# Performance work log

Hardware: AMD Instinct MI355X
Metric: run time of the kernel (lower is better)

## Reference

```python
import jax, jax.numpy as jnp
import numpy as np

B, T, C = 4, 2048, 1024
H = 16
DH = C // H  # 64


def setup_inputs() -> dict:
    key = jax.random.key(0)
    ks = jax.random.split(key, 6)
    s = 1.0 / np.sqrt(C)
    x = jax.random.normal(ks[0], (B, T, C), dtype=jnp.float32)
    # per-head projection weights, stacked: (H, C, DH)
    Wq = jax.random.uniform(ks[1], (H, C, DH), dtype=jnp.float32, minval=-s, maxval=s)
    Wk = jax.random.uniform(ks[2], (H, C, DH), dtype=jnp.float32, minval=-s, maxval=s)
    Wv = jax.random.uniform(ks[3], (H, C, DH), dtype=jnp.float32, minval=-s, maxval=s)
    # output projection (torch Linear: y = x @ W.T + b); store as (C, C) for x @ Wo
    Wo = jax.random.uniform(ks[4], (C, C), dtype=jnp.float32, minval=-s, maxval=s)
    bo = jax.random.uniform(ks[5], (C,), dtype=jnp.float32, minval=-s, maxval=s)
    return {"x": x, "Wq": Wq, "Wk": Wk, "Wv": Wv, "Wo": Wo, "bo": bo}


def reference(x, Wq, Wk, Wv, Wo, bo):
    # x: (B,T,C) -> q,k,v: (B,H,T,DH)
    q = jnp.einsum('btc,hcd->bhtd', x, Wq)
    k = jnp.einsum('btc,hcd->bhtd', x, Wk)
    v = jnp.einsum('btc,hcd->bhtd', x, Wv)
    scale = DH ** -0.5
    scores = jnp.einsum('bhtd,bhsd->bhts', q, k) * scale  # (B,H,T,T)
    causal = jnp.tril(jnp.ones((T, T), dtype=bool))
    scores = jnp.where(causal, scores, -jnp.inf)
    wei = jax.nn.softmax(scores, axis=-1)
    out = jnp.einsum('bhts,bhsd->bhtd', wei, v)  # (B,H,T,DH)
    # concat heads: (B,T,H*DH) = (B,T,C)
    out = out.transpose(0, 2, 1, 3).reshape(B, T, C)
    return out @ Wo + bo
```

## Files before the change

kernel.cpp:

```cpp
#include <hip/hip_runtime.h>

#define T_SEQ 2048
#define C_DIM 1024
#define H_NUM 16
#define DHD   64
#define B_NUM 4
#define M_ROWS (B_NUM*T_SEQ)

typedef __bf16 bf16x8 __attribute__((ext_vector_type(8)));
typedef float  f32x4  __attribute__((ext_vector_type(4)));
typedef unsigned short ushort8 __attribute__((ext_vector_type(8)));
typedef unsigned short ushort4e __attribute__((ext_vector_type(4)));

__device__ __forceinline__ unsigned short f2b(float f){
  return __builtin_bit_cast(unsigned short, (__bf16)f);
}
__device__ __forceinline__ bf16x8 as_bf(ushort8 u){ return __builtin_bit_cast(bf16x8, u); }
__device__ __forceinline__ float exp2fast(float x){ return __builtin_amdgcn_exp2f(x); }

__device__ __forceinline__ void gload16(const void* g, void* l){
  __builtin_amdgcn_global_load_lds(
      (const __attribute__((address_space(1))) void*)g,
      (__attribute__((address_space(3))) void*)l, 16, 0, 0);
}

__global__ __launch_bounds__(256) void k_conv_x(const float* __restrict__ x,
                                                unsigned short* __restrict__ xb){
  int i = blockIdx.x*256 + threadIdx.x;
  float4 f = ((const float4*)x)[i];
  ushort4e o;
  o[0]=f2b(f.x); o[1]=f2b(f.y); o[2]=f2b(f.z); o[3]=f2b(f.w);
  ((ushort4e*)xb)[i] = o;
}

__global__ __launch_bounds__(256) void k_pack_w(const float* __restrict__ wq,
                                                const float* __restrict__ wk,
                                                const float* __restrict__ wv,
                                                const float* __restrict__ wo,
                                                unsigned short* __restrict__ wt,
                                                unsigned short* __restrict__ wot){
  int idx = blockIdx.x*256 + threadIdx.x;
  if (idx < 3*C_DIM*C_DIM){
    int nall = idx >> 10; int c = idx & 1023;
    int m = nall >> 10;   int n = nall & 1023;
    int h = n >> 6, d = n & 63;
    const float* w = (m==0) ? wq : (m==1) ? wk : wv;
    float f = w[((size_t)h*C_DIM + c)*DHD + d];
    if (m == 0) f *= 0.125f * 1.4426950408889634f;
    wt[idx] = f2b(f);
  } else {
    int j = idx - 3*C_DIM*C_DIM;
    int n = j >> 10, c = j & 1023;
    wot[j] = f2b(wo[(size_t)c*C_DIM + n]);
  }
}

__global__ __launch_bounds__(256) void k_gemm_qkv(const unsigned short* __restrict__ xb,
                                                  const unsigned short* __restrict__ wt,
                                                  unsigned short* __restrict__ qo,
                                                  unsigned short* __restrict__ ko,
                                                  unsigned short* __restrict__ vo){
  __shared__ __align__(16) unsigned short a_lds[128*64];
  __shared__ __align__(16) unsigned short b_lds[128*64];
  const int tid = threadIdx.x, lane = tid & 63, wid = tid >> 6;
  const int g = lane >> 4, tl = lane & 15;
  const int wr = wid >> 1, wc = wid & 1;
  const int id = blockIdx.x;
  const int swz = (id & 7)*192 + (id >> 3);
  const int mbase = (swz / 24) * 128, nbase = (swz % 24) * 128;
  f32x4 acc[4][4] = {};
  for (int kk = 0; kk < C_DIM; kk += 64){
    __syncthreads();
    #pragma unroll
    for (int i = 0; i < 4; i++){
      const int brow = (wid*4 + i)*8;
      const int row  = brow + (lane >> 3);
      const int jj   = (lane & 7) ^ (row & 7);
      gload16(&xb[(size_t)(mbase+row)*C_DIM + kk + jj*8], &a_lds[brow*64]);
      gload16(&wt[(size_t)(nbase+row)*C_DIM + kk + jj*8], &b_lds[brow*64]);
    }
    __syncthreads();
    bf16x8 aF[4][2], bF[4][2];
    #pragma unroll
    for (int mb = 0; mb < 4; mb++){
      const int row = wr*64 + mb*16 + tl; const int s7 = row & 7;
      aF[mb][0] = as_bf(*(const ushort8*)&a_lds[row*64 + ((g     ^ s7)*8)]);
      aF[mb][1] = as_bf(*(const ushort8*)&a_lds[row*64 + (((4+g) ^ s7)*8)]);
    }
    #pragma unroll
    for (int nb = 0; nb < 4; nb++){
      const int row = wc*64 + nb*16 + tl; const int s7 = row & 7;
      bF[nb][0] = as_bf(*(const ushort8*)&b_lds[row*64 + ((g     ^ s7)*8)]);
      bF[nb][1] = as_bf(*(const ushort8*)&b_lds[row*64 + (((4+g) ^ s7)*8)]);
    }
    #pragma unroll
    for (int mb = 0; mb < 4; mb++)
      #pragma unroll
      for (int nb = 0; nb < 4; nb++){
        acc[mb][nb] = __builtin_amdgcn_mfma_f32_16x16x32_bf16(aF[mb][0], bF[nb][0], acc[mb][nb], 0,0,0);
        acc[mb][nb] = __builtin_amdgcn_mfma_f32_16x16x32_bf16(aF[mb][1], bF[nb][1], acc[mb][nb], 0,0,0);
      }
  }
  #pragma unroll
  for (int mb = 0; mb < 4; mb++){
    #pragma unroll
    for (int nb = 0; nb < 4; nb++){
      #pragma unroll
      for (int r = 0; r < 4; r++){
        int gr = mbase + wr*64 + mb*16 + g*4 + r;
        int gc = nbase + wc*64 + nb*16 + tl;
        int b = gr >> 11, t = gr & 2047;
        int sel = gc >> 10, nw = gc & 1023;
        int h = nw >> 6, d = nw & 63;
        unsigned short* dst = (sel == 0) ? qo : (sel == 1) ? ko : vo;
        dst[(((size_t)(b*H_NUM + h))*T_SEQ + t)*DHD + d] = f2b(acc[mb][nb][r]);
      }
    }
  }
}

__global__ __launch_bounds__(256) void k_tr_v(const unsigned short* __restrict__ vsrc,
                                              unsigned short* __restrict__ vdst){
  __shared__ __align__(16) unsigned short vr[64][72];
  int tid = threadIdx.x;
  int bh = blockIdx.y; int tbase = blockIdx.x * 64;
  const unsigned short* vb = vsrc + (size_t)bh * T_SEQ * DHD;
  unsigned short* vo = vdst + (size_t)bh * DHD * T_SEQ;
  #pragma unroll
  for (int i = 0; i < 2; i++){
    int id = tid + i*256;
    int row = id >> 3, c8 = (id & 7) << 3;
    *(ushort8*)&vr[row][c8 ^ ((row >> 3) << 3)] =
        *(const ushort8*)&vb[(size_t)(tbase + row)*DHD + c8];
  }
  __syncthreads();
  #pragma unroll
  for (int i = 0; i < 2; i++){
    int id = tid + i*256;
    int d = id >> 3, oc = id & 7;
    ushort8 out;
    #pragma unroll
    for (int j = 0; j < 8; j++){
      int t = oc*8 + j;
      out[j] = vr[t][d ^ (oc << 3)];
    }
    *(ushort8*)&vo[(size_t)d*T_SEQ + tbase + oc*8] = out;
  }
}

__global__ __launch_bounds__(512) void k_flash(const unsigned short* __restrict__ q,
                                               const unsigned short* __restrict__ k,
                                               const unsigned short* __restrict__ vtg,
                                               unsigned short* __restrict__ o){
  __shared__ __align__(16) unsigned short kbufs[2][64*64];
  __shared__ __align__(16) unsigned short vbufs[2][64*64];
  __shared__ __align__(16) unsigned short pl[8][32][72];
  const int tid = threadIdx.x, lane = tid & 63, w = tid >> 6;
  const int g = lane >> 4, tl = lane & 15;
  const int id = blockIdx.x;
  const int swz = (id & 7)*32 + (id >> 3);
  const int bh = swz >> 2, bx = swz & 3;
  const int b = bh >> 4, h = bh & 15;
  const unsigned short* qb = q   + (size_t)bh * T_SEQ * DHD;
  const unsigned short* kb = k   + (size_t)bh * T_SEQ * DHD;
  const unsigned short* vb = vtg + (size_t)bh * (size_t)DHD * T_SEQ;
  const int lrow = lane >> 3, lj = lane & 7;

  for (int pass = 0; pass < 2; ++pass){
    const int qt = pass ? (7 - bx) : bx;
    const int tbase = qt * 256;
    const int trow0 = tbase + w * 32;
    const int tmax = trow0 + 31;
    bf16x8 qF[2][2];
    #pragma unroll
    for (int tf = 0; tf < 2; tf++)
      #pragma unroll
      for (int ks = 0; ks < 2; ks++)
        qF[tf][ks] = as_bf(*(const ushort8*)&qb[(size_t)(trow0 + tf*16 + tl)*DHD + ks*32 + g*8]);
    f32x4 acc[2][4] = {};
    float mreg[2] = {-1e30f, -1e30f}, lreg[2] = {0.f, 0.f};
    const int nkt = 4*qt + 4;
    {
      const int row = w*8 + lrow;
      const int jj = lj ^ (row & 7);
      gload16(&kb[(size_t)row*DHD + jj*8],   &kbufs[0][w*8*64]);
      gload16(&vb[(size_t)row*T_SEQ + jj*8], &vbufs[0][w*8*64]);
    }
    __syncthreads();
    for (int kti = 0; kti < nkt; ++kti){
      const int cur = kti & 1;
      const int kbase = kti * 64;
      if (kti + 1 < nkt){
        const int kb2 = kbase + 64;
        const int row = w*8 + lrow;
        const int jj = lj ^ (row & 7);
        gload16(&kb[(size_t)(kb2+row)*DHD + jj*8],   &kbufs[cur^1][w*8*64]);
        gload16(&vb[(size_t)row*T_SEQ + kb2 + jj*8], &vbufs[cur^1][w*8*64]);
      }
      if (kbase <= tmax){
        const unsigned short* kcur = kbufs[cur];
        const unsigned short* vcur = vbufs[cur];
        const int s7 = tl & 7;
        f32x4 st[2][4] = {};
        __builtin_amdgcn_s_setprio(1);
        #pragma unroll
        for (int sf = 0; sf < 4; sf++){
          const int row = sf*16 + tl;
          bf16x8 kf0 = as_bf(*(const ushort8*)&kcur[row*64 + ((g     ^ s7)*8)]);
          bf16x8 kf1 = as_bf(*(const ushort8*)&kcur[row*64 + (((4+g) ^ s7)*8)]);
          #pragma unroll
          for (int tf = 0; tf < 2; tf++){
            st[tf][sf] = __builtin_amdgcn_mfma_f32_16x16x32_bf16(kf0, qF[tf][0], st[tf][sf], 0,0,0);
            st[tf][sf] = __builtin_amdgcn_mfma_f32_16x16x32_bf16(kf1, qF[tf][1], st[tf][sf], 0,0,0);
          }
        }
        __builtin_amdgcn_s_setprio(0);
        if (kbase + 63 > trow0){
          #pragma unroll
          for (int tf = 0; tf < 2; tf++){
            int tg = trow0 + tf*16 + tl;
            #pragma unroll
            for (int sf = 0; sf < 4; sf++)
              #pragma unroll
              for (int r = 0; r < 4; r++)
                if (kbase + sf*16 + g*4 + r > tg) st[tf][sf][r] = -1e30f;
          }
        }
        #pragma unroll
        for (int tf = 0; tf < 2; tf++){
          float mloc = -1e30f;
          #pragma unroll
          for (int sf = 0; sf < 4; sf++)
            #pragma unroll
            for (int r = 0; r < 4; r++) mloc = fmaxf(mloc, st[tf][sf][r]);
          mloc = fmaxf(mloc, __shfl_xor(mloc, 16));
          mloc = fmaxf(mloc, __shfl_xor(mloc, 32));
          if (__any(mloc > mreg[tf] + 8.f)){
            float mnew = fmaxf(mreg[tf], mloc);
            float alpha = exp2fast(mreg[tf] - mnew);
            mreg[tf] = mnew;
            lreg[tf] *= alpha;
            #pragma unroll
            for (int df = 0; df < 4; df++)
              #pragma unroll
              for (int r = 0; r < 4; r++) acc[tf][df][r] *= alpha;
          }
          float sum = 0.f;
          #pragma unroll
          for (int sf = 0; sf < 4; sf++){
            ushort4e pk;
            #pragma unroll
            for (int r = 0; r < 4; r++){
              float p = exp2fast(st[tf][sf][r] - mreg[tf]);
              sum += p;
              pk[r] = f2b(p);
            }
            *(ushort4e*)&pl[w][tf*16 + tl][sf*16 + g*4] = pk;
          }
          sum += __shfl_xor(sum, 16);
          sum += __shfl_xor(sum, 32);
          lreg[tf] += sum;
        }
        bf16x8 pa[2][2];
        #pragma unroll
        for (int tf = 0; tf < 2; tf++)
          #pragma unroll
          for (int ks = 0; ks < 2; ks++)
            pa[tf][ks] = as_bf(*(const ushort8*)&pl[w][tf*16 + tl][ks*32 + g*8]);
        __builtin_amdgcn_s_setprio(1);
        #pragma unroll
        for (int df = 0; df < 4; df++){
          const int row = df*16 + tl;
          bf16x8 vf0 = as_bf(*(const ushort8*)&vcur[row*64 + ((g     ^ s7)*8)]);
          bf16x8 vf1 = as_bf(*(const ushort8*)&vcur[row*64 + (((4+g) ^ s7)*8)]);
          #pragma unroll
          for (int tf = 0; tf < 2; tf++){
            acc[tf][df] = __builtin_amdgcn_mfma_f32_16x16x32_bf16(vf0, pa[tf][0], acc[tf][df], 0,0,0);
            acc[tf][df] = __builtin_amdgcn_mfma_f32_16x16x32_bf16(vf1, pa[tf][1], acc[tf][df], 0,0,0);
          }
        }
        __builtin_amdgcn_s_setprio(0);
      }
      __syncthreads();
    }
    #pragma unroll
    for (int tf = 0; tf < 2; tf++){
      float inv = 1.f / lreg[tf];
      int tg = trow0 + tf*16 + tl;
      #pragma unroll
      for (int df = 0; df < 4; df++){
        ushort4e ov;
        #pragma unroll
        for (int r = 0; r < 4; r++) ov[r] = f2b(acc[tf][df][r] * inv);
        *(ushort4e*)&o[((size_t)(b*T_SEQ + tg))*C_DIM + h*DHD + df*16 + g*4] = ov;
      }
    }
  }
}

__global__ __launch_bounds__(256) void k_gemm_proj(const unsigned short* __restrict__ ab,
                                                   const unsigned short* __restrict__ wot,
                                                   const float* __restrict__ bo,
                                                   float* __restrict__ out){
  __shared__ __align__(16) unsigned short a_lds[128*64];
  __shared__ __align__(16) unsigned short b_lds[128*64];
  const int tid = threadIdx.x, lane = tid & 63, wid = tid >> 6;
  const int g = lane >> 4, tl = lane & 15;
  const int wr = wid >> 1, wc = wid & 1;
  const int id = blockIdx.x;
  const int swz = (id & 7)*64 + (id >> 3);
  const int mbase = (swz >> 3) * 128, nbase = (swz & 7) * 128;
  f32x4 acc[4][4] = {};
  for (int kk = 0; kk < C_DIM; kk += 64){
    __syncthreads();
    #pragma unroll
    for (int i = 0; i < 4; i++){
      const int brow = (wid*4 + i)*8;
      const int row  = brow + (lane >> 3);
      const int jj   = (lane & 7) ^ (row & 7);
      gload16(&ab[(size_t)(mbase+row)*C_DIM + kk + jj*8],  &a_lds[brow*64]);
      gload16(&wot[(size_t)(nbase+row)*C_DIM + kk + jj*8], &b_lds[brow*64]);
    }
    __syncthreads();
    bf16x8 aF[4][2], bF[4][2];
    #pragma unroll
    for (int mb = 0; mb < 4; mb++){
      const int row = wr*64 + mb*16 + tl; const int s7 = row & 7;
      aF[mb][0] = as_bf(*(const ushort8*)&a_lds[row*64 + ((g     ^ s7)*8)]);
      aF[mb][1] = as_bf(*(const ushort8*)&a_lds[row*64 + (((4+g) ^ s7)*8)]);
    }
    #pragma unroll
    for (int nb = 0; nb < 4; nb++){
      const int row = wc*64 + nb*16 + tl; const int s7 = row & 7;
      bF[nb][0] = as_bf(*(const ushort8*)&b_lds[row*64 + ((g     ^ s7)*8)]);
      bF[nb][1] = as_bf(*(const ushort8*)&b_lds[row*64 + (((4+g) ^ s7)*8)]);
    }
    #pragma unroll
    for (int mb = 0; mb < 4; mb++)
      #pragma unroll
      for (int nb = 0; nb < 4; nb++){
        acc[mb][nb] = __builtin_amdgcn_mfma_f32_16x16x32_bf16(aF[mb][0], bF[nb][0], acc[mb][nb], 0,0,0);
        acc[mb][nb] = __builtin_amdgcn_mfma_f32_16x16x32_bf16(aF[mb][1], bF[nb][1], acc[mb][nb], 0,0,0);
      }
  }
  #pragma unroll
  for (int mb = 0; mb < 4; mb++){
    #pragma unroll
    for (int nb = 0; nb < 4; nb++){
      #pragma unroll
      for (int r = 0; r < 4; r++){
        int gr = mbase + wr*64 + mb*16 + g*4 + r;
        int gc = nbase + wc*64 + nb*16 + tl;
        out[(size_t)gr*C_DIM + gc] = acc[mb][nb][r] + bo[gc];
      }
    }
  }
}

extern "C" void kernel_launch(void* const* d_in, const int* in_sizes, int n_in,
                              void* d_out, int out_size, void* d_ws, size_t ws_size,
                              hipStream_t stream){
  const float* x  = (const float*)d_in[0];
  const float* Wq = (const float*)d_in[1];
  const float* Wk = (const float*)d_in[2];
  const float* Wv = (const float*)d_in[3];
  const float* Wo = (const float*)d_in[4];
  const float* bo = (const float*)d_in[5];
  float* out = (float*)d_out;

  char* p = (char*)d_ws;
  unsigned short* xb  = (unsigned short*)p; p += (size_t)M_ROWS*C_DIM*2;
  unsigned short* wt  = (unsigned short*)p; p += (size_t)3*C_DIM*C_DIM*2;
  unsigned short* wot = (unsigned short*)p; p += (size_t)C_DIM*C_DIM*2;
  unsigned short* Qb  = (unsigned short*)p; p += (size_t)M_ROWS*C_DIM*2;
  unsigned short* Kb  = (unsigned short*)p; p += (size_t)M_ROWS*C_DIM*2;
  unsigned short* Vb  = (unsigned short*)p; p += (size_t)M_ROWS*C_DIM*2;
  unsigned short* Vtr  = xb;
  unsigned short* attn = Vb;

  hipLaunchKernelGGL(k_conv_x, dim3(M_ROWS*C_DIM/4/256), dim3(256), 0, stream, x, xb);
  hipLaunchKernelGGL(k_pack_w, dim3(4*C_DIM*C_DIM/256), dim3(256), 0, stream,
                     Wq, Wk, Wv, Wo, wt, wot);
  hipLaunchKernelGGL(k_gemm_qkv, dim3(1536), dim3(256), 0, stream,
                     xb, wt, Qb, Kb, Vb);
  hipLaunchKernelGGL(k_tr_v, dim3(T_SEQ/64, B_NUM*H_NUM), dim3(256), 0, stream, Vb, Vtr);
  hipLaunchKernelGGL(k_flash, dim3(256), dim3(512), 0, stream,
                     Qb, Kb, Vtr, attn);
  hipLaunchKernelGGL(k_gemm_proj, dim3(512), dim3(256), 0, stream,
                     attn, wot, bo, out);
}
```

Baseline: 191.2 us.

## Fuse V transpose into QKV GEMM epilogue and defer softmax row reductions

The QKV GEMM now writes V directly in transposed (d-major) layout through an LDS staging tile in its epilogue. This removes the separate transpose kernel and its extra global round trip of V. The flash kernel also drops the per-tile cross-lane shuffles for the row max and row sum, doing the max shuffle only when a rescale is triggered and summing partial l values across lanes once at the end. The rescale check now uses the per-lane max, which may trigger rescales more often, and the workspace aliasing changes so attention output reuses the x buffer.

```diff
diff --git a/kernel.cpp b/kernel.cpp
--- a/kernel.cpp
+++ b/kernel.cpp
@@ -59,9 +59,8 @@
                                                   const unsigned short* __restrict__ wt,
                                                   unsigned short* __restrict__ qo,
                                                   unsigned short* __restrict__ ko,
-                                                  unsigned short* __restrict__ vo){
-  __shared__ __align__(16) unsigned short a_lds[128*64];
-  __shared__ __align__(16) unsigned short b_lds[128*64];
+                                                  unsigned short* __restrict__ vtr){
+  __shared__ __align__(16) unsigned short smem[2][128*64];
   const int tid = threadIdx.x, lane = tid & 63, wid = tid >> 6;
   const int g = lane >> 4, tl = lane & 15;
   const int wr = wid >> 1, wc = wid & 1;
@@ -76,22 +75,22 @@
       const int brow = (wid*4 + i)*8;
       const int row  = brow + (lane >> 3);
       const int jj   = (lane & 7) ^ (row & 7);
-      gload16(&xb[(size_t)(mbase+row)*C_DIM + kk + jj*8], &a_lds[brow*64]);
-      gload16(&wt[(size_t)(nbase+row)*C_DIM + kk + jj*8], &b_lds[brow*64]);
+      gload16(&xb[(size_t)(mbase+row)*C_DIM + kk + jj*8], &smem[0][brow*64]);
+      gload16(&wt[(size_t)(nbase+row)*C_DIM + kk + jj*8], &smem[1][brow*64]);
     }
     __syncthreads();
     bf16x8 aF[4][2], bF[4][2];
     #pragma unroll
     for (int mb = 0; mb < 4; mb++){
       const int row = wr*64 + mb*16 + tl; const int s7 = row & 7;
-      aF[mb][0] = as_bf(*(const ushort8*)&a_lds[row*64 + ((g     ^ s7)*8)]);
-      aF[mb][1] = as_bf(*(const ushort8*)&a_lds[row*64 + (((4+g) ^ s7)*8)]);
+      aF[mb][0] = as_bf(*(const ushort8*)&smem[0][row*64 + ((g     ^ s7)*8)]);
+      aF[mb][1] = as_bf(*(const ushort8*)&smem[0][row*64 + (((4+g) ^ s7)*8)]);
     }
     #pragma unroll
     for (int nb = 0; nb < 4; nb++){
       const int row = wc*64 + nb*16 + tl; const int s7 = row & 7;
-      bF[nb][0] = as_bf(*(const ushort8*)&b_lds[row*64 + ((g     ^ s7)*8)]);
-      bF[nb][1] = as_bf(*(const ushort8*)&b_lds[row*64 + (((4+g) ^ s7)*8)]);
+      bF[nb][0] = as_bf(*(const ushort8*)&smem[1][row*64 + ((g     ^ s7)*8)]);
+      bF[nb][1] = as_bf(*(const ushort8*)&smem[1][row*64 + (((4+g) ^ s7)*8)]);
     }
     #pragma unroll
     for (int mb = 0; mb < 4; mb++)
@@ -101,50 +100,50 @@
         acc[mb][nb] = __builtin_amdgcn_mfma_f32_16x16x32_bf16(aF[mb][1], bF[nb][1], acc[mb][nb], 0,0,0);
       }
   }
-  #pragma unroll
-  for (int mb = 0; mb < 4; mb++){
-    #pragma unroll
-    for (int nb = 0; nb < 4; nb++){
-      #pragma unroll
-      for (int r = 0; r < 4; r++){
-        int gr = mbase + wr*64 + mb*16 + g*4 + r;
-        int gc = nbase + wc*64 + nb*16 + tl;
-        int b = gr >> 11, t = gr & 2047;
-        int sel = gc >> 10, nw = gc & 1023;
-        int h = nw >> 6, d = nw & 63;
-        unsigned short* dst = (sel == 0) ? qo : (sel == 1) ? ko : vo;
-        dst[(((size_t)(b*H_NUM + h))*T_SEQ + t)*DHD + d] = f2b(acc[mb][nb][r]);
-      }
-    }
-  }
-}
-
-__global__ __launch_bounds__(256) void k_tr_v(const unsigned short* __restrict__ vsrc,
-                                              unsigned short* __restrict__ vdst){
-  __shared__ __align__(16) unsigned short vr[64][72];
-  int tid = threadIdx.x;
-  int bh = blockIdx.y; int tbase = blockIdx.x * 64;
-  const unsigned short* vb = vsrc + (size_t)bh * T_SEQ * DHD;
-  unsigned short* vo = vdst + (size_t)bh * DHD * T_SEQ;
-  #pragma unroll
-  for (int i = 0; i < 2; i++){
-    int id = tid + i*256;
-    int row = id >> 3, c8 = (id & 7) << 3;
-    *(ushort8*)&vr[row][c8 ^ ((row >> 3) << 3)] =
-        *(const ushort8*)&vb[(size_t)(tbase + row)*DHD + c8];
-  }
-  __syncthreads();
-  #pragma unroll
-  for (int i = 0; i < 2; i++){
-    int id = tid + i*256;
-    int d = id >> 3, oc = id & 7;
-    ushort8 out;
-    #pragma unroll
-    for (int j = 0; j < 8; j++){
-      int t = oc*8 + j;
-      out[j] = vr[t][d ^ (oc << 3)];
-    }
-    *(ushort8*)&vo[(size_t)d*T_SEQ + tbase + oc*8] = out;
+  const int sel = nbase >> 10;
+  if (sel < 2){
+    unsigned short* dst0 = (sel == 0) ? qo : ko;
+    #pragma unroll
+    for (int mb = 0; mb < 4; mb++){
+      #pragma unroll
+      for (int nb = 0; nb < 4; nb++){
+        #pragma unroll
+        for (int r = 0; r < 4; r++){
+          int gr = mbase + wr*64 + mb*16 + g*4 + r;
+          int gc = nbase + wc*64 + nb*16 + tl;
+          int b = gr >> 11, t = gr & 2047;
+          int nw = gc & 1023;
+          int h = nw >> 6, d = nw & 63;
+          dst0[(((size_t)(b*H_NUM + h))*T_SEQ + t)*DHD + d] = f2b(acc[mb][nb][r]);
+        }
+      }
+    }
+  } else {
+    __syncthreads();
+    unsigned short* tr = &smem[0][0];
+    #pragma unroll
+    for (int mb = 0; mb < 4; mb++){
+      #pragma unroll
+      for (int nb = 0; nb < 4; nb++){
+        const int n = wc*64 + nb*16 + tl;
+        const int m0 = wr*64 + mb*16 + g*4;
+        ushort4e pk;
+        #pragma unroll
+        for (int r = 0; r < 4; r++) pk[r] = f2b(acc[mb][nb][r]);
+        *(ushort4e*)&tr[n*128 + (m0 ^ ((n & 15) << 3))] = pk;
+      }
+    }
+    __syncthreads();
+    const int hbase = (nbase - 2048) >> 6;
+    const int b = mbase >> 11, tloc = mbase & 2047;
+    const int n = tid >> 1, half = tid & 1;
+    unsigned short* vdst = vtr + (((size_t)(b*H_NUM + hbase + (n >> 6)))*DHD + (n & 63))*T_SEQ
+                           + tloc + half*64;
+    #pragma unroll
+    for (int c8 = 0; c8 < 8; c8++){
+      const int chunk = (half*8 + c8) ^ (n & 15);
+      *(ushort8*)&vdst[c8*8] = *(const ushort8*)&tr[n*128 + chunk*8];
+    }
   }
 }
 
@@ -233,10 +232,10 @@
           for (int sf = 0; sf < 4; sf++)
             #pragma unroll
             for (int r = 0; r < 4; r++) mloc = fmaxf(mloc, st[tf][sf][r]);
-          mloc = fmaxf(mloc, __shfl_xor(mloc, 16));
-          mloc = fmaxf(mloc, __shfl_xor(mloc, 32));
           if (__any(mloc > mreg[tf] + 8.f)){
-            float mnew = fmaxf(mreg[tf], mloc);
+            float mrow = fmaxf(mloc, __shfl_xor(mloc, 16));
+            mrow = fmaxf(mrow, __shfl_xor(mrow, 32));
+            float mnew = fmaxf(mreg[tf], mrow);
             float alpha = exp2fast(mreg[tf] - mnew);
             mreg[tf] = mnew;
             lreg[tf] *= alpha;
@@ -257,8 +256,6 @@
             }
             *(ushort4e*)&pl[w][tf*16 + tl][sf*16 + g*4] = pk;
           }
-          sum += __shfl_xor(sum, 16);
-          sum += __shfl_xor(sum, 32);
           lreg[tf] += sum;
         }
         bf16x8 pa[2][2];
@@ -285,7 +282,10 @@
     }
     #pragma unroll
     for (int tf = 0; tf < 2; tf++){
-      float inv = 1.f / lreg[tf];
+      float l = lreg[tf];
+      l += __shfl_xor(l, 16);
+      l += __shfl_xor(l, 32);
+      float inv = 1.f / l;
       int tg = trow0 + tf*16 + tl;
       #pragma unroll
       for (int df = 0; df < 4; df++){
@@ -374,16 +374,14 @@
   unsigned short* wot = (unsigned short*)p; p += (size_t)C_DIM*C_DIM*2;
   unsigned short* Qb  = (unsigned short*)p; p += (size_t)M_ROWS*C_DIM*2;
   unsigned short* Kb  = (unsigned short*)p; p += (size_t)M_ROWS*C_DIM*2;
-  unsigned short* Vb  = (unsigned short*)p; p += (size_t)M_ROWS*C_DIM*2;
-  unsigned short* Vtr  = xb;
-  unsigned short* attn = Vb;
+  unsigned short* Vtr = (unsigned short*)p; p += (size_t)M_ROWS*C_DIM*2;
+  unsigned short* attn = xb;
 
   hipLaunchKernelGGL(k_conv_x, dim3(M_ROWS*C_DIM/4/256), dim3(256), 0, stream, x, xb);
   hipLaunchKernelGGL(k_pack_w, dim3(4*C_DIM*C_DIM/256), dim3(256), 0, stream,
                      Wq, Wk, Wv, Wo, wt, wot);
   hipLaunchKernelGGL(k_gemm_qkv, dim3(1536), dim3(256), 0, stream,
-                     xb, wt, Qb, Kb, Vb);
-  hipLaunchKernelGGL(k_tr_v, dim3(T_SEQ/64, B_NUM*H_NUM), dim3(256), 0, stream, Vb, Vtr);
+                     xb, wt, Qb, Kb, Vtr);
   hipLaunchKernelGGL(k_flash, dim3(256), dim3(512), 0, stream,
                      Qb, Kb, Vtr, attn);
   hipLaunchKernelGGL(k_gemm_proj, dim3(512), dim3(256), 0, stream,
```

Measured after the change: 183.3 us. -4.1%, faster.

## Rewrite QKV GEMM as 256x256 double-buffered 8-wave pipelined kernel; defer softmax row reductions

Applied to the files above, without the earlier changes.

Replaces the 128x128 single-buffered QKV GEMM with a 256x256 tile, 8-wave kernel that double-buffers A and B in LDS and interleaves global-to-LDS loads with MFMA phases using explicit waitcnt and barriers. This is meant to hide load latency and raise reuse per tile, at the cost of much more LDS and register pressure. In the flash kernel, the cross-lane shuffles for the row max are now done only when a rescale is triggered, and the row-sum shuffles are moved to the final normalization, trimming per-tile shuffle work.

```diff
diff --git a/kernel.cpp b/kernel.cpp
--- a/kernel.cpp
+++ b/kernel.cpp
@@ -23,6 +23,8 @@
       (const __attribute__((address_space(1))) void*)g,
       (__attribute__((address_space(3))) void*)l, 16, 0, 0);
 }
+
+#define MF(a,b,c) __builtin_amdgcn_mfma_f32_16x16x32_bf16(a,b,c,0,0,0)
 
 __global__ __launch_bounds__(256) void k_conv_x(const float* __restrict__ x,
                                                 unsigned short* __restrict__ xb){
@@ -55,65 +57,100 @@
   }
 }
 
-__global__ __launch_bounds__(256) void k_gemm_qkv(const unsigned short* __restrict__ xb,
-                                                  const unsigned short* __restrict__ wt,
+__global__ __launch_bounds__(512, 2) void k_gemm8(const unsigned short* __restrict__ gA,
+                                                  const unsigned short* __restrict__ gB,
                                                   unsigned short* __restrict__ qo,
                                                   unsigned short* __restrict__ ko,
                                                   unsigned short* __restrict__ vo){
-  __shared__ __align__(16) unsigned short a_lds[128*64];
-  __shared__ __align__(16) unsigned short b_lds[128*64];
+  __shared__ __align__(16) unsigned short aS[2][256*64];
+  __shared__ __align__(16) unsigned short bS[2][256*64];
   const int tid = threadIdx.x, lane = tid & 63, wid = tid >> 6;
   const int g = lane >> 4, tl = lane & 15;
-  const int wr = wid >> 1, wc = wid & 1;
+  const int wm = wid >> 2, wn = wid & 3;
+  const int wmb = wm*128, wnb = wn*64;
   const int id = blockIdx.x;
-  const int swz = (id & 7)*192 + (id >> 3);
-  const int mbase = (swz / 24) * 128, nbase = (swz % 24) * 128;
-  f32x4 acc[4][4] = {};
-  for (int kk = 0; kk < C_DIM; kk += 64){
-    __syncthreads();
-    #pragma unroll
-    for (int i = 0; i < 4; i++){
-      const int brow = (wid*4 + i)*8;
-      const int row  = brow + (lane >> 3);
-      const int jj   = (lane & 7) ^ (row & 7);
-      gload16(&xb[(size_t)(mbase+row)*C_DIM + kk + jj*8], &a_lds[brow*64]);
-      gload16(&wt[(size_t)(nbase+row)*C_DIM + kk + jj*8], &b_lds[brow*64]);
-    }
-    __syncthreads();
-    bf16x8 aF[4][2], bF[4][2];
-    #pragma unroll
-    for (int mb = 0; mb < 4; mb++){
-      const int row = wr*64 + mb*16 + tl; const int s7 = row & 7;
-      aF[mb][0] = as_bf(*(const ushort8*)&a_lds[row*64 + ((g     ^ s7)*8)]);
-      aF[mb][1] = as_bf(*(const ushort8*)&a_lds[row*64 + (((4+g) ^ s7)*8)]);
-    }
-    #pragma unroll
-    for (int nb = 0; nb < 4; nb++){
-      const int row = wc*64 + nb*16 + tl; const int s7 = row & 7;
-      bF[nb][0] = as_bf(*(const ushort8*)&b_lds[row*64 + ((g     ^ s7)*8)]);
-      bF[nb][1] = as_bf(*(const ushort8*)&b_lds[row*64 + (((4+g) ^ s7)*8)]);
-    }
-    #pragma unroll
-    for (int mb = 0; mb < 4; mb++)
-      #pragma unroll
-      for (int nb = 0; nb < 4; nb++){
-        acc[mb][nb] = __builtin_amdgcn_mfma_f32_16x16x32_bf16(aF[mb][0], bF[nb][0], acc[mb][nb], 0,0,0);
-        acc[mb][nb] = __builtin_amdgcn_mfma_f32_16x16x32_bf16(aF[mb][1], bF[nb][1], acc[mb][nb], 0,0,0);
-      }
-  }
+  const int swz = (id & 7)*48 + (id >> 3);
+  const int mbase = (swz / 12) * 256, nbase = (swz % 12) * 256;
+  const int srow = tid >> 3;
+  const int jj   = (((tid & 7) ^ (srow & 7)) * 8);
+  const int jdst = (tid & 7) * 8;
+  const int c0 = ((g     ^ (tl & 7)) * 8);
+  const int c1 = (((4+g) ^ (tl & 7)) * 8);
+
+#define SA(S, KT, RB) gload16(&gA[(size_t)(mbase + (RB) + srow)*C_DIM + (KT)*64 + jj], \
+                              &aS[S][((RB) + srow)*64 + jdst])
+#define SB(S, KT, RB) gload16(&gB[(size_t)(nbase + (RB) + srow)*C_DIM + (KT)*64 + jj], \
+                              &bS[S][((RB) + srow)*64 + jdst])
+
+#define GPHASE(S, Q, STAGES, TAIL) do{                                         \
+  const int rA0 = (wmb + (2*(Q))*16 + tl)*64, rA1 = rA0 + 16*64;               \
+  bf16x8 aE0 = as_bf(*(const ushort8*)&aS[S][rA0 + c0]);                       \
+  bf16x8 aE1 = as_bf(*(const ushort8*)&aS[S][rA0 + c1]);                       \
+  bf16x8 aO0 = as_bf(*(const ushort8*)&aS[S][rA1 + c0]);                       \
+  bf16x8 aO1 = as_bf(*(const ushort8*)&aS[S][rA1 + c1]);                       \
+  if ((Q) == 0){                                                               \
+    _Pragma("unroll")                                                          \
+    for (int nf = 0; nf < 4; nf++){                                            \
+      const int rB = (wnb + nf*16 + tl)*64;                                    \
+      bF[nf][0] = as_bf(*(const ushort8*)&bS[S][rB + c0]);                     \
+      bF[nf][1] = as_bf(*(const ushort8*)&bS[S][rB + c1]);                     \
+    }                                                                          \
+  }                                                                            \
+  STAGES                                                                       \
+  asm volatile("s_barrier" ::: "memory");                                      \
+  __builtin_amdgcn_s_setprio(1);                                               \
+  _Pragma("unroll")                                                            \
+  for (int nf = 0; nf < 4; nf++){                                              \
+    acc[2*(Q)][nf]   = MF(aE0, bF[nf][0], acc[2*(Q)][nf]);                     \
+    acc[2*(Q)][nf]   = MF(aE1, bF[nf][1], acc[2*(Q)][nf]);                     \
+    acc[2*(Q)+1][nf] = MF(aO0, bF[nf][0], acc[2*(Q)+1][nf]);                   \
+    acc[2*(Q)+1][nf] = MF(aO1, bF[nf][1], acc[2*(Q)+1][nf]);                   \
+  }                                                                            \
+  __builtin_amdgcn_s_setprio(0);                                               \
+  TAIL                                                                         \
+  asm volatile("s_barrier" ::: "memory");                                      \
+}while(0)
+
+  f32x4 acc[8][4] = {};
+  SA(0,0,0); SA(0,0,64); SA(0,0,128); SA(0,0,192);
+  SB(0,0,0); SB(0,0,64); SB(0,0,128); SB(0,0,192);
+  SB(1,1,0); SB(1,1,64); SB(1,1,128); SB(1,1,192);
+  asm volatile("s_waitcnt vmcnt(4)" ::: "memory");
+  asm volatile("s_barrier" ::: "memory");
+
+  #pragma unroll 1
+  for (int i = 0; i < 8; ++i){
+    const int u = 2*i; const bool nl = (i < 7);
+    bf16x8 bF[4][2];
+    GPHASE(0, 0, SA(1, u+1, 0); SA(1, u+1, 64); , );
+    GPHASE(0, 1, SA(1, u+1, 128); SA(1, u+1, 192); , );
+    GPHASE(0, 2, if (nl){ SB(0, u+2, 0); SB(0, u+2, 64); } , );
+    GPHASE(0, 3, if (nl){ SB(0, u+2, 128); SB(0, u+2, 192); } ,
+           if (nl) asm volatile("s_waitcnt vmcnt(4)" ::: "memory");
+           else    asm volatile("s_waitcnt vmcnt(0)" ::: "memory"); );
+    GPHASE(1, 0, if (nl){ SA(0, u+2, 0); SA(0, u+2, 64); } , );
+    GPHASE(1, 1, if (nl){ SA(0, u+2, 128); SA(0, u+2, 192); } , );
+    GPHASE(1, 2, if (nl){ SB(1, u+3, 0); SB(1, u+3, 64); } , );
+    GPHASE(1, 3, if (nl){ SB(1, u+3, 128); SB(1, u+3, 192); } ,
+           if (nl) asm volatile("s_waitcnt vmcnt(4)" ::: "memory"); );
+  }
+#undef GPHASE
+#undef SA
+#undef SB
+
+  const int sel = nbase >> 10;
+  unsigned short* dst = (sel == 0) ? qo : (sel == 1) ? ko : vo;
   #pragma unroll
-  for (int mb = 0; mb < 4; mb++){
-    #pragma unroll
-    for (int nb = 0; nb < 4; nb++){
+  for (int mf = 0; mf < 8; mf++){
+    #pragma unroll
+    for (int nf = 0; nf < 4; nf++){
       #pragma unroll
       for (int r = 0; r < 4; r++){
-        int gr = mbase + wr*64 + mb*16 + g*4 + r;
-        int gc = nbase + wc*64 + nb*16 + tl;
+        int gr = mbase + wmb + mf*16 + g*4 + r;
+        int gc = nbase + wnb + nf*16 + tl;
         int b = gr >> 11, t = gr & 2047;
-        int sel = gc >> 10, nw = gc & 1023;
-        int h = nw >> 6, d = nw & 63;
-        unsigned short* dst = (sel == 0) ? qo : (sel == 1) ? ko : vo;
-        dst[(((size_t)(b*H_NUM + h))*T_SEQ + t)*DHD + d] = f2b(acc[mb][nb][r]);
+        int nw = gc & 1023, h = nw >> 6, d = nw & 63;
+        dst[(((size_t)(b*H_NUM + h))*T_SEQ + t)*DHD + d] = f2b(acc[mf][nf][r]);
       }
     }
   }
@@ -210,8 +247,8 @@
           bf16x8 kf1 = as_bf(*(const ushort8*)&kcur[row*64 + (((4+g) ^ s7)*8)]);
           #pragma unroll
           for (int tf = 0; tf < 2; tf++){
-            st[tf][sf] = __builtin_amdgcn_mfma_f32_16x16x32_bf16(kf0, qF[tf][0], st[tf][sf], 0,0,0);
-            st[tf][sf] = __builtin_amdgcn_mfma_f32_16x16x32_bf16(kf1, qF[tf][1], st[tf][sf], 0,0,0);
+            st[tf][sf] = MF(kf0, qF[tf][0], st[tf][sf]);
+            st[tf][sf] = MF(kf1, qF[tf][1], st[tf][sf]);
           }
         }
         __builtin_amdgcn_s_setprio(0);
@@ -233,10 +270,10 @@
           for (int sf = 0; sf < 4; sf++)
             #pragma unroll
             for (int r = 0; r < 4; r++) mloc = fmaxf(mloc, st[tf][sf][r]);
-          mloc = fmaxf(mloc, __shfl_xor(mloc, 16));
-          mloc = fmaxf(mloc, __shfl_xor(mloc, 32));
           if (__any(mloc > mreg[tf] + 8.f)){
-            float mnew = fmaxf(mreg[tf], mloc);
+            float mrow = fmaxf(mloc, __shfl_xor(mloc, 16));
+            mrow = fmaxf(mrow, __shfl_xor(mrow, 32));
+            float mnew = fmaxf(mreg[tf], mrow);
             float alpha = exp2fast(mreg[tf] - mnew);
             mreg[tf] = mnew;
             lreg[tf] *= alpha;
@@ -257,8 +294,6 @@
             }
             *(ushort4e*)&pl[w][tf*16 + tl][sf*16 + g*4] = pk;
           }
-          sum += __shfl_xor(sum, 16);
-          sum += __shfl_xor(sum, 32);
           lreg[tf] += sum;
         }
         bf16x8 pa[2][2];
@@ -275,8 +310,8 @@
           bf16x8 vf1 = as_bf(*(const ushort8*)&vcur[row*64 + (((4+g) ^ s7)*8)]);
           #pragma unroll
           for (int tf = 0; tf < 2; tf++){
-            acc[tf][df] = __builtin_amdgcn_mfma_f32_16x16x32_bf16(vf0, pa[tf][0], acc[tf][df], 0,0,0);
-            acc[tf][df] = __builtin_amdgcn_mfma_f32_16x16x32_bf16(vf1, pa[tf][1], acc[tf][df], 0,0,0);
+            acc[tf][df] = MF(vf0, pa[tf][0], acc[tf][df]);
+            acc[tf][df] = MF(vf1, pa[tf][1], acc[tf][df]);
           }
         }
         __builtin_amdgcn_s_setprio(0);
@@ -285,7 +320,10 @@
     }
     #pragma unroll
     for (int tf = 0; tf < 2; tf++){
-      float inv = 1.f / lreg[tf];
+      float l = lreg[tf];
+      l += __shfl_xor(l, 16);
+      l += __shfl_xor(l, 32);
+      float inv = 1.f / l;
       int tg = trow0 + tf*16 + tl;
       #pragma unroll
       for (int df = 0; df < 4; df++){
@@ -339,8 +377,8 @@
     for (int mb = 0; mb < 4; mb++)
       #pragma unroll
       for (int nb = 0; nb < 4; nb++){
-        acc[mb][nb] = __builtin_amdgcn_mfma_f32_16x16x32_bf16(aF[mb][0], bF[nb][0], acc[mb][nb], 0,0,0);
-        acc[mb][nb] = __builtin_amdgcn_mfma_f32_16x16x32_bf16(aF[mb][1], bF[nb][1], acc[mb][nb], 0,0,0);
+        acc[mb][nb] = MF(aF[mb][0], bF[nb][0], acc[mb][nb]);
+        acc[mb][nb] = MF(aF[mb][1], bF[nb][1], acc[mb][nb]);
       }
   }
   #pragma unroll
@@ -381,7 +419,7 @@
   hipLaunchKernelGGL(k_conv_x, dim3(M_ROWS*C_DIM/4/256), dim3(256), 0, stream, x, xb);
   hipLaunchKernelGGL(k_pack_w, dim3(4*C_DIM*C_DIM/256), dim3(256), 0, stream,
                      Wq, Wk, Wv, Wo, wt, wot);
-  hipLaunchKernelGGL(k_gemm_qkv, dim3(1536), dim3(256), 0, stream,
+  hipLaunchKernelGGL(k_gemm8, dim3(384), dim3(512), 0, stream,
                      xb, wt, Qb, Kb, Vb);
   hipLaunchKernelGGL(k_tr_v, dim3(T_SEQ/64, B_NUM*H_NUM), dim3(256), 0, stream, Vb, Vtr);
   hipLaunchKernelGGL(k_flash, dim3(256), dim3(512), 0, stream,
```

New measurement: 187.3 us. 1.02x faster.
